# Performance work log

Measured on AMD Instinct MI355X. Metric: run time of the kernel, lower is better.

Reference implementation:

```python
import jax, jax.numpy as jnp
import numpy as np

B, N, F = 32, 64, 128   # batch, nodes, input features (F == hidden_dim)
E = N * (N - 1)         # fully-connected directed edges = 4032
H, D = 4, 64            # heads, out_dim per head
ALPHA = 0.2             # leaky relu slope


def setup_inputs() -> dict:
    key = jax.random.key(0)
    ks = jax.random.split(key, 16)
    v_self = jax.random.normal(ks[0], (B, N, F), dtype=jnp.float32)
    # fully-connected one-hot sender/receiver matrices [E, N], broadcast to [B, E, N]
    pairs = np.array([(i, j) for i in range(N) for j in range(N) if i != j])
    send = np.zeros((E, N), np.float32); send[np.arange(E), pairs[:, 0]] = 1.0
    rec = np.zeros((E, N), np.float32); rec[np.arange(E), pairs[:, 1]] = 1.0
    rel_send = jnp.broadcast_to(jnp.asarray(send), (B, E, N))
    rel_rec = jnp.broadcast_to(jnp.asarray(rec), (B, E, N))
    s = 0.05
    return {
        "v_self": v_self,
        "rel_rec": rel_rec,
        "rel_send": rel_send,
        "W_proj": jax.random.normal(ks[1], (H * D, F), dtype=jnp.float32) * s,
        "a_fwd": jax.random.normal(ks[2], (H, D), dtype=jnp.float32) * s,
        "a_bwd": jax.random.normal(ks[3], (H, D), dtype=jnp.float32) * s,
        "We1": jax.random.normal(ks[4], (D, 2 * D), dtype=jnp.float32) * s,
        "be1": jnp.zeros((D,), jnp.float32),
        "We2": jax.random.normal(ks[5], (D, D), dtype=jnp.float32) * s,
        "be2": jnp.zeros((D,), jnp.float32),
        "Wv1": jax.random.normal(ks[6], (F, D), dtype=jnp.float32) * s,
        "bv1": jnp.zeros((F,), jnp.float32),
        "Wv2": jax.random.normal(ks[7], (F, F), dtype=jnp.float32) * s,
        "bv2": jnp.zeros((F,), jnp.float32),
        "Wv3": jax.random.normal(ks[8], (D, F), dtype=jnp.float32) * s,
        "bv3": jnp.zeros((D,), jnp.float32),
    }


def _leaky(x):
    return jnp.where(x >= 0, x, ALPHA * x)


def reference(v_self, rel_rec, rel_send, W_proj, a_fwd, a_bwd,
              We1, be1, We2, be2, Wv1, bv1, Wv2, bv2, Wv3, bv3):
    # project: [B,N,F] -> [B,N,H,D]
    v_proj = (v_self @ W_proj.T).reshape(B, N, H, D)
    # gather to edges via one-hot adjacency (v_src==h_src, v_tgt==h_tgt in original)
    h_src = jnp.einsum('ben,bnhd->behd', rel_send, v_proj)
    h_tgt = jnp.einsum('ben,bnhd->behd', rel_rec, v_proj)
    attn_ij = _leaky(jnp.einsum('behd,hd->beh', h_src, a_fwd)) / 500.0
    attn_ji = _leaky(jnp.einsum('behd,hd->beh', h_tgt, a_bwd)) / 500.0
    attn_max = jnp.maximum(attn_ij, attn_ji)
    # NOTE: original applies exp twice (exp of exp); reproduced faithfully
    e_ij = jnp.exp(jnp.exp(attn_ij - attn_max))
    e_ji = jnp.exp(jnp.exp(attn_ji - attn_max))
    alpha_sum = e_ij + e_ji
    alpha_ij = e_ij / alpha_sum   # [B,E,H]
    alpha_ji = e_ji / alpha_sum
    edge_input = jnp.concatenate(
        [alpha_ij[..., None] * h_src, alpha_ji[..., None] * h_tgt], axis=-1)  # [B,E,H,2D]
    # f_CG_e: Linear(2D->D), ReLU, Linear(D->D) on last dim
    e_cg = jax.nn.relu(edge_input @ We1.T + be1) @ We2.T + be2
    edge_weighted = e_cg * alpha_ij[..., None]                               # [B,E,H,D]
    # scatter back to nodes
    v_social = jnp.einsum('behd,ben->bnhd', edge_weighted, rel_rec)          # [B,N,H,D]
    # f_CG_v: Linear(D->F), ReLU, Linear(F->F), ReLU, Linear(F->D)
    x = jax.nn.relu(v_social @ Wv1.T + bv1)
    x = jax.nn.relu(x @ Wv2.T + bv2)
    x = x @ Wv3.T + bv3
    v_out = x.reshape(B, N, H * D)  # concat_heads=True
    return (v_out, alpha_ij)
```

## Files before the change

kernel.cpp:

```cpp
#include <hip/hip_runtime.h>

#define B_ 32
#define N_ 64
#define F_ 128
#define E_ 4032
#define H_ 4
#define D_ 64

typedef __bf16 bf16x8 __attribute__((ext_vector_type(8)));
typedef __bf16 bf16x4 __attribute__((ext_vector_type(4)));
typedef float  f32x4  __attribute__((ext_vector_type(4)));


__global__ __launch_bounds__(256) void k_proj(
    const float* __restrict__ v_self, const float* __restrict__ W_proj,
    const float* __restrict__ We1,
    const float* __restrict__ a_fwd, const float* __restrict__ a_bwd,
    const float* __restrict__ Wv1, const float* __restrict__ We2,
    const float* __restrict__ be2, const float* __restrict__ Wv2,
    const float* __restrict__ Wv3,
    float* __restrict__ s_fwd, float* __restrict__ s_bwd,
    __bf16* __restrict__ u_src, __bf16* __restrict__ u_tgt,
    __bf16* __restrict__ M1bf, float* __restrict__ wb,
    __bf16* __restrict__ Wv2bf, __bf16* __restrict__ Wv3bf)
{
    const int t = threadIdx.x;

    if (blockIdx.x >= B_ * N_ / 8) {
        const int pid = (blockIdx.x - B_ * N_ / 8) * 256 + t;
        const int f = pid >> 6, k = pid & 63;
        float acc = 0.f;
        for (int dd = 0; dd < 64; ++dd)
            acc += Wv1[f * 64 + dd] * We2[dd * 64 + k];
        M1bf[pid] = (__bf16)acc;
        float p = Wv1[f * 64 + k] * be2[k];
#pragma unroll
        for (int m = 1; m < 64; m <<= 1) p += __shfl_xor(p, m);
        if (k == 0) wb[f] = p;
        Wv2bf[pid]        = (__bf16)Wv2[pid];
        Wv2bf[pid + 8192] = (__bf16)Wv2[pid + 8192];
        Wv3bf[pid]        = (__bf16)Wv3[pid];
        return;
    }

    const int w = t >> 6, l = t & 63;
    const int q = l >> 4, lr = l & 15;
    const int node0 = blockIdx.x * 8;

    __shared__ __bf16 Av[16 * 136];
    __shared__ __bf16 P_lds[8 * 288];

    {
        int row = t >> 5, c0 = (t & 31) * 4;
        float4 v = *(const float4*)(v_self + (size_t)(node0 + row) * 128 + c0);
        bf16x4 bv; bv[0]=(__bf16)v.x; bv[1]=(__bf16)v.y; bv[2]=(__bf16)v.z; bv[3]=(__bf16)v.w;
        *(bf16x4*)&Av[row * 136 + c0] = bv;
        bf16x4 z = {};
        *(bf16x4*)&Av[(row + 8) * 136 + c0] = z;
    }
    __syncthreads();

    f32x4 acc[4] = {};
#pragma unroll
    for (int ks = 0; ks < 4; ++ks) {
        bf16x8 a = *(const bf16x8*)&Av[lr * 136 + ks * 32 + q * 8];
#pragma unroll
        for (int ct = 0; ct < 4; ++ct) {
            const float4* wr = (const float4*)(W_proj + (size_t)(w * 64 + ct * 16 + lr) * 128 + ks * 32 + q * 8);
            float4 w0 = wr[0], w1 = wr[1];
            bf16x8 b;
            b[0]=(__bf16)w0.x; b[1]=(__bf16)w0.y; b[2]=(__bf16)w0.z; b[3]=(__bf16)w0.w;
            b[4]=(__bf16)w1.x; b[5]=(__bf16)w1.y; b[6]=(__bf16)w1.z; b[7]=(__bf16)w1.w;
            acc[ct] = __builtin_amdgcn_mfma_f32_16x16x32_bf16(a, b, acc[ct], 0, 0, 0);
        }
    }

    {
        float pf[4] = {0,0,0,0}, pb[4] = {0,0,0,0};
#pragma unroll
        for (int ct = 0; ct < 4; ++ct) {
            float af = a_fwd[w * 64 + ct * 16 + lr];
            float ab = a_bwd[w * 64 + ct * 16 + lr];
#pragma unroll
            for (int r = 0; r < 4; ++r) { pf[r] += acc[ct][r] * af; pb[r] += acc[ct][r] * ab; }
        }
#pragma unroll
        for (int m = 1; m < 16; m <<= 1) {
#pragma unroll
            for (int r = 0; r < 4; ++r) { pf[r] += __shfl_xor(pf[r], m); pb[r] += __shfl_xor(pb[r], m); }
        }
        if (lr == 0 && q < 2) {
#pragma unroll
            for (int r = 0; r < 4; ++r) {
                int node = q * 4 + r;
                float x = pf[r]; x = (x >= 0.f ? x : 0.2f * x) * 0.002f;
                float y = pb[r]; y = (y >= 0.f ? y : 0.2f * y) * 0.002f;
                s_fwd[(node0 + node) * 4 + w] = x;
                s_bwd[(node0 + node) * 4 + w] = y;
            }
        }
    }
    if (q < 2) {
#pragma unroll
        for (int ct = 0; ct < 4; ++ct)
#pragma unroll
            for (int r = 0; r < 4; ++r)
                P_lds[(q * 4 + r) * 288 + w * 72 + ct * 16 + lr] = (__bf16)acc[ct][r];
    }
    __syncthreads();

    const int rt = w & 1, mm = w >> 1;
    const int rr = rt * 16 + lr, an = rr >> 2, ah = rr & 3;
    f32x4 uacc[4] = {};
#pragma unroll
    for (int ks = 0; ks < 2; ++ks) {
        bf16x8 a = *(const bf16x8*)&P_lds[an * 288 + ah * 72 + ks * 32 + q * 8];
#pragma unroll
        for (int ct = 0; ct < 4; ++ct) {
            const float4* wr = (const float4*)(We1 + (size_t)(ct * 16 + lr) * 128 + mm * 64 + ks * 32 + q * 8);
            float4 w0 = wr[0], w1 = wr[1];
            bf16x8 b;
            b[0]=(__bf16)w0.x; b[1]=(__bf16)w0.y; b[2]=(__bf16)w0.z; b[3]=(__bf16)w0.w;
            b[4]=(__bf16)w1.x; b[5]=(__bf16)w1.y; b[6]=(__bf16)w1.z; b[7]=(__bf16)w1.w;
            uacc[ct] = __builtin_amdgcn_mfma_f32_16x16x32_bf16(a, b, uacc[ct], 0, 0, 0);
        }
    }
    __bf16* up = (mm == 0) ? u_src : u_tgt;
#pragma unroll
    for (int ct = 0; ct < 4; ++ct)
#pragma unroll
        for (int r = 0; r < 4; ++r) {
            int row = rt * 16 + q * 4 + r;
            up[(size_t)(node0 * 4 + row) * 64 + ct * 16 + lr] = (__bf16)uacc[ct][r];
        }
}

__global__ __launch_bounds__(256) void k_fused(
    const float* __restrict__ s_fwd, const float* __restrict__ s_bwd,
    const __bf16* __restrict__ u_src, const __bf16* __restrict__ u_tgt,
    const float* __restrict__ be1,
    const __bf16* __restrict__ M1bf, const float* __restrict__ wb,
    const float* __restrict__ bv1,
    const __bf16* __restrict__ Wv2bf, const float* __restrict__ bv2,
    const __bf16* __restrict__ Wv3bf, const float* __restrict__ bv3,
    float* __restrict__ v_out, float* __restrict__ out_alpha)
{
    const int t = threadIdx.x;
    const int h = t >> 6, d = t & 63;
    const int b = blockIdx.x >> 3, oct = blockIdx.x & 7;
    const int j0 = oct * 8;

    __shared__ float u_l[4][64][64];
    __shared__ float ut_l[8][4][64];
    __shared__ float aij_l[4][64][8];
    __shared__ float suma_l[32];
    __shared__ __bf16 g_l[32 * 72];

    {
        const __bf16* ub = u_src + (size_t)b * 16384;
        for (int idx = t * 8; idx < 16384; idx += 256 * 8) {
            bf16x8 v = *(const bf16x8*)(ub + idx);
            int i = idx >> 8, col = idx & 255;
            float* dst = &u_l[col >> 6][i][col & 63];
#pragma unroll
            for (int z = 0; z < 8; ++z) dst[z] = (float)v[z];
        }
        const __bf16* utp = u_tgt + ((size_t)(b * 64 + j0)) * 256;
        {
            int idx = t * 8;
            bf16x8 v = *(const bf16x8*)(utp + idx);
            int j = idx >> 8, col = idx & 255;
            float* dst = &ut_l[j][col >> 6][col & 63];
#pragma unroll
            for (int z = 0; z < 8; ++z) dst[z] = (float)v[z];
        }
    }

    {
        const int i = d;
        float sfi = s_fwd[(b * 64 + i) * 4 + h];
        float areg[8];
#pragma unroll
        for (int j = 0; j < 8; ++j) {
            float sbj = s_bwd[(b * 64 + j0 + j) * 4 + h];
            float m = fmaxf(sfi, sbj);
            float eij = __expf(__expf(sfi - m));
            float eji = __expf(__expf(sbj - m));
            float aij = eij / (eij + eji);
            if (i == j0 + j) aij = 0.f;
            areg[j] = aij;
        }
        f32x4 a0 = {areg[0], areg[1], areg[2], areg[3]};
        f32x4 a1 = {areg[4], areg[5], areg[6], areg[7]};
        *(f32x4*)&aij_l[h][i][0] = a0;
        *(f32x4*)&aij_l[h][i][4] = a1;
#pragma unroll
        for (int j = 0; j < 8; ++j) {
            float sa = areg[j];
#pragma unroll
            for (int m2 = 1; m2 < 64; m2 <<= 1) sa += __shfl_xor(sa, m2);
            if (i == 0) suma_l[j * 4 + h] = sa;
        }
    }
    if (t < 252) {
        const int jj = t >> 2, h2 = t & 3;
#pragma unroll
        for (int s = 0; s < 8; ++s) {
            int i2 = j0 + s;
            int j2 = jj + (jj >= i2 ? 1 : 0);
            float sfi = s_fwd[(b * 64 + i2) * 4 + h2];
            float sbj = s_bwd[(b * 64 + j2) * 4 + h2];
            float m = fmaxf(sfi, sbj);
            float eij = __expf(__expf(sfi - m));
            float eji = __expf(__expf(sbj - m));
            out_alpha[((size_t)b * E_ + i2 * 63 + jj) * 4 + h2] = eij / (eij + eji);
        }
    }
    __syncthreads();

    {
        const float be1d = be1[d];
        float utv[8], utb[8];
#pragma unroll
        for (int j = 0; j < 8; ++j) { utv[j] = ut_l[j][h][d]; utb[j] = utv[j] + be1d; }
        float gacc[8] = {};
        for (int i = 0; i < 64; ++i) {
            float usv = u_l[h][i][d];
            f32x4 a0 = *(const f32x4*)&aij_l[h][i][0];
            f32x4 a1 = *(const f32x4*)&aij_l[h][i][4];
#pragma unroll
            for (int j = 0; j < 4; ++j) {
                float a = a0[j];
                float hp = fmaf(a, usv - utv[j], utb[j]);
                gacc[j] = fmaf(a, fmaxf(hp, 0.f), gacc[j]);
                float a2 = a1[j];
                float hp2 = fmaf(a2, usv - utv[4 + j], utb[4 + j]);
                gacc[4 + j] = fmaf(a2, fmaxf(hp2, 0.f), gacc[4 + j]);
            }
        }
#pragma unroll
        for (int j = 0; j < 8; ++j)
            g_l[(j * 4 + h) * 72 + d] = (__bf16)gacc[j];
    }
    __syncthreads();

    __bf16* X1 = (__bf16*)&u_l[0][0][0];
    __bf16* X2 = X1 + 32 * 136;
    const int w = h, l = t & 63;
    const int q = l >> 4, lr = l & 15;
    const int rt = w & 1, ch = w >> 1;
    const int rows_base = (b * 64 + j0) * 4;

    f32x4 acc1[4] = {};
#pragma unroll
    for (int ks = 0; ks < 2; ++ks) {
        bf16x8 a = *(const bf16x8*)&g_l[(rt * 16 + lr) * 72 + ks * 32 + q * 8];
#pragma unroll
        for (int ct = 0; ct < 4; ++ct) {
            bf16x8 bfr = *(const bf16x8*)(M1bf + (size_t)(ch * 64 + ct * 16 + lr) * 64 + ks * 32 + q * 8);
            acc1[ct] = __builtin_amdgcn_mfma_f32_16x16x32_bf16(a, bfr, acc1[ct], 0, 0, 0);
        }
    }
    float sml[4];
#pragma unroll
    for (int r = 0; r < 4; ++r) sml[r] = suma_l[rt * 16 + q * 4 + r];
#pragma unroll
    for (int ct = 0; ct < 4; ++ct) {
        int f = ch * 64 + ct * 16 + lr;
        float wbf = wb[f], b1 = bv1[f];
#pragma unroll
        for (int r = 0; r < 4; ++r) {
            float xv = acc1[ct][r] + sml[r] * wbf + b1;
            X1[(rt * 16 + q * 4 + r) * 136 + f] = (__bf16)fmaxf(xv, 0.f);
        }
    }
    __syncthreads();

    f32x4 acc2[4] = {};
#pragma unroll
    for (int ks = 0; ks < 4; ++ks) {
        bf16x8 a = *(const bf16x8*)&X1[(rt * 16 + lr) * 136 + ks * 32 + q * 8];
#pragma unroll
        for (int ct = 0; ct < 4; ++ct) {
            bf16x8 bfr = *(const bf16x8*)(Wv2bf + (size_t)(ch * 64 + ct * 16 + lr) * 128 + ks * 32 + q * 8);
            acc2[ct] = __builtin_amdgcn_mfma_f32_16x16x32_bf16(a, bfr, acc2[ct], 0, 0, 0);
        }
    }
#pragma unroll
    for (int ct = 0; ct < 4; ++ct) {
        int f = ch * 64 + ct * 16 + lr;
        float b2 = bv2[f];
#pragma unroll
        for (int r = 0; r < 4; ++r) {
            float xv = acc2[ct][r] + b2;
            X2[(rt * 16 + q * 4 + r) * 136 + f] = (__bf16)fmaxf(xv, 0.f);
        }
    }
    __syncthreads();

    f32x4 acc3[2] = {};
#pragma unroll
    for (int ks = 0; ks < 4; ++ks) {
        bf16x8 a = *(const bf16x8*)&X2[(rt * 16 + lr) * 136 + ks * 32 + q * 8];
#pragma unroll
        for (int ct = 0; ct < 2; ++ct) {
            bf16x8 bfr = *(const bf16x8*)(Wv3bf + (size_t)(ch * 32 + ct * 16 + lr) * 128 + ks * 32 + q * 8);
            acc3[ct] = __builtin_amdgcn_mfma_f32_16x16x32_bf16(a, bfr, acc3[ct], 0, 0, 0);
        }
    }
#pragma unroll
    for (int ct = 0; ct < 2; ++ct) {
        int dd = ch * 32 + ct * 16 + lr;
        float b3 = bv3[dd];
#pragma unroll
        for (int r = 0; r < 4; ++r)
            v_out[(size_t)(rows_base + rt * 16 + q * 4 + r) * 64 + dd] = acc3[ct][r] + b3;
    }
}

extern "C" void kernel_launch(void* const* d_in, const int* in_sizes, int n_in,
                              void* d_out, int out_size, void* d_ws, size_t ws_size,
                              hipStream_t stream) {
    (void)in_sizes; (void)n_in; (void)out_size; (void)ws_size;
    const float* v_self = (const float*)d_in[0];
    const float* W_proj = (const float*)d_in[3];
    const float* a_fwd  = (const float*)d_in[4];
    const float* a_bwd  = (const float*)d_in[5];
    const float* We1    = (const float*)d_in[6];
    const float* be1    = (const float*)d_in[7];
    const float* We2    = (const float*)d_in[8];
    const float* be2    = (const float*)d_in[9];
    const float* Wv1    = (const float*)d_in[10];
    const float* bv1    = (const float*)d_in[11];
    const float* Wv2    = (const float*)d_in[12];
    const float* bv2    = (const float*)d_in[13];
    const float* Wv3    = (const float*)d_in[14];
    const float* bv3    = (const float*)d_in[15];

    float* ws = (float*)d_ws;
    float*  s_fwd = ws;
    float*  s_bwd = ws + 8192;
    float*  wb    = ws + 24576;
    __bf16* M1bf  = (__bf16*)(ws + 24704);
    __bf16* Wv2bf = (__bf16*)(ws + 28800);
    __bf16* Wv3bf = (__bf16*)(ws + 36992);
    __bf16* u_src = (__bf16*)(ws + 61568);
    __bf16* u_tgt = (__bf16*)(ws + 323712);

    float* v_out = (float*)d_out;
    float* alpha = v_out + (size_t)B_ * N_ * H_ * D_;

    hipLaunchKernelGGL(k_proj, dim3(B_ * N_ / 8 + 32), dim3(256), 0, stream,
                       v_self, W_proj, We1, a_fwd, a_bwd, Wv1, We2, be2, Wv2, Wv3,
                       s_fwd, s_bwd, u_src, u_tgt, M1bf, wb, Wv2bf, Wv3bf);
    hipLaunchKernelGGL(k_fused, dim3(B_ * N_ / 8), dim3(256), 0, stream,
                       s_fwd, s_bwd, u_src, u_tgt, be1, M1bf, wb, bv1,
                       Wv2bf, bv2, Wv3bf, bv3, v_out, alpha);
}
```

Before: 31.43 us.

## Repartition both kernels into smaller blocks and read u_src directly from global

k_proj now runs single-wave 64-thread blocks, each handling 16 nodes and one head. Each block computes both the u_src and u_tgt halves of We1, and the wasted zero-padded rows are dropped. k_fused handles 4 targets per block instead of 8, doubling the grid to 512 blocks, and streams u_src from global memory in bf16 instead of staging a 64 KB fp32 copy in LDS. The intent is to cut LDS use so more blocks fit per CU, and to fill the GPU better; the cost is redundant global reads of u_src across more blocks and less reuse per block.

Result: faster. 29.11 us (-7.4%).

```diff
diff --git a/kernel.cpp b/kernel.cpp
--- a/kernel.cpp
+++ b/kernel.cpp
@@ -12,7 +12,15 @@
 typedef float  f32x4  __attribute__((ext_vector_type(4)));
 
 
-__global__ __launch_bounds__(256) void k_proj(
+static __device__ inline bf16x8 ld_cvt8(const float* __restrict__ p) {
+    float4 w0 = *(const float4*)p, w1 = *(const float4*)(p + 4);
+    bf16x8 b;
+    b[0]=(__bf16)w0.x; b[1]=(__bf16)w0.y; b[2]=(__bf16)w0.z; b[3]=(__bf16)w0.w;
+    b[4]=(__bf16)w1.x; b[5]=(__bf16)w1.y; b[6]=(__bf16)w1.z; b[7]=(__bf16)w1.w;
+    return b;
+}
+
+__global__ __launch_bounds__(64) void k_proj(
     const float* __restrict__ v_self, const float* __restrict__ W_proj,
     const float* __restrict__ We1,
     const float* __restrict__ a_fwd, const float* __restrict__ a_bwd,
@@ -25,10 +33,12 @@
     __bf16* __restrict__ Wv2bf, __bf16* __restrict__ Wv3bf)
 {
     const int t = threadIdx.x;
-
-    if (blockIdx.x >= B_ * N_ / 8) {
-        const int pid = (blockIdx.x - B_ * N_ / 8) * 256 + t;
-        const int f = pid >> 6, k = pid & 63;
+    const int blk = blockIdx.x;
+
+    if (blk >= 512) {
+        const int f = blk - 512;
+        const int k = t;
+        const int pid = f * 64 + k;
         float acc = 0.f;
         for (int dd = 0; dd < 64; ++dd)
             acc += Wv1[f * 64 + dd] * We2[dd * 64 + k];
@@ -43,35 +53,20 @@
         return;
     }
 
-    const int w = t >> 6, l = t & 63;
-    const int q = l >> 4, lr = l & 15;
-    const int node0 = blockIdx.x * 8;
-
-    __shared__ __bf16 Av[16 * 136];
-    __shared__ __bf16 P_lds[8 * 288];
-
-    {
-        int row = t >> 5, c0 = (t & 31) * 4;
-        float4 v = *(const float4*)(v_self + (size_t)(node0 + row) * 128 + c0);
-        bf16x4 bv; bv[0]=(__bf16)v.x; bv[1]=(__bf16)v.y; bv[2]=(__bf16)v.z; bv[3]=(__bf16)v.w;
-        *(bf16x4*)&Av[row * 136 + c0] = bv;
-        bf16x4 z = {};
-        *(bf16x4*)&Av[(row + 8) * 136 + c0] = z;
-    }
-    __syncthreads();
+    const int tile = blk >> 2, w = blk & 3;
+    const int node0 = tile * 16;
+    const int q = t >> 4, lr = t & 15;
+
+    __shared__ __bf16 P_lds[16 * 72];
 
     f32x4 acc[4] = {};
 #pragma unroll
     for (int ks = 0; ks < 4; ++ks) {
-        bf16x8 a = *(const bf16x8*)&Av[lr * 136 + ks * 32 + q * 8];
+        bf16x8 a = ld_cvt8(v_self + (size_t)(node0 + lr) * 128 + ks * 32 + q * 8);
 #pragma unroll
         for (int ct = 0; ct < 4; ++ct) {
-            const float4* wr = (const float4*)(W_proj + (size_t)(w * 64 + ct * 16 + lr) * 128 + ks * 32 + q * 8);
-            float4 w0 = wr[0], w1 = wr[1];
-            bf16x8 b;
-            b[0]=(__bf16)w0.x; b[1]=(__bf16)w0.y; b[2]=(__bf16)w0.z; b[3]=(__bf16)w0.w;
-            b[4]=(__bf16)w1.x; b[5]=(__bf16)w1.y; b[6]=(__bf16)w1.z; b[7]=(__bf16)w1.w;
-            acc[ct] = __builtin_amdgcn_mfma_f32_16x16x32_bf16(a, b, acc[ct], 0, 0, 0);
+            bf16x8 bb = ld_cvt8(W_proj + (size_t)(w * 64 + ct * 16 + lr) * 128 + ks * 32 + q * 8);
+            acc[ct] = __builtin_amdgcn_mfma_f32_16x16x32_bf16(a, bb, acc[ct], 0, 0, 0);
         }
     }
 
@@ -89,49 +84,43 @@
 #pragma unroll
             for (int r = 0; r < 4; ++r) { pf[r] += __shfl_xor(pf[r], m); pb[r] += __shfl_xor(pb[r], m); }
         }
-        if (lr == 0 && q < 2) {
+        if (lr == 0) {
 #pragma unroll
             for (int r = 0; r < 4; ++r) {
-                int node = q * 4 + r;
                 float x = pf[r]; x = (x >= 0.f ? x : 0.2f * x) * 0.002f;
                 float y = pb[r]; y = (y >= 0.f ? y : 0.2f * y) * 0.002f;
-                s_fwd[(node0 + node) * 4 + w] = x;
-                s_bwd[(node0 + node) * 4 + w] = y;
+                s_fwd[(node0 + q * 4 + r) * 4 + w] = x;
+                s_bwd[(node0 + q * 4 + r) * 4 + w] = y;
             }
         }
     }
-    if (q < 2) {
-#pragma unroll
-        for (int ct = 0; ct < 4; ++ct)
-#pragma unroll
-            for (int r = 0; r < 4; ++r)
-                P_lds[(q * 4 + r) * 288 + w * 72 + ct * 16 + lr] = (__bf16)acc[ct][r];
-    }
-    __syncthreads();
-
-    const int rt = w & 1, mm = w >> 1;
-    const int rr = rt * 16 + lr, an = rr >> 2, ah = rr & 3;
-    f32x4 uacc[4] = {};
+
+#pragma unroll
+    for (int ct = 0; ct < 4; ++ct)
+#pragma unroll
+        for (int r = 0; r < 4; ++r)
+            P_lds[(q * 4 + r) * 72 + ct * 16 + lr] = (__bf16)acc[ct][r];
+    __syncthreads();
+
+    f32x4 us[4] = {}, ut[4] = {};
 #pragma unroll
     for (int ks = 0; ks < 2; ++ks) {
-        bf16x8 a = *(const bf16x8*)&P_lds[an * 288 + ah * 72 + ks * 32 + q * 8];
+        bf16x8 a = *(const bf16x8*)&P_lds[lr * 72 + ks * 32 + q * 8];
 #pragma unroll
         for (int ct = 0; ct < 4; ++ct) {
-            const float4* wr = (const float4*)(We1 + (size_t)(ct * 16 + lr) * 128 + mm * 64 + ks * 32 + q * 8);
-            float4 w0 = wr[0], w1 = wr[1];
-            bf16x8 b;
-            b[0]=(__bf16)w0.x; b[1]=(__bf16)w0.y; b[2]=(__bf16)w0.z; b[3]=(__bf16)w0.w;
-            b[4]=(__bf16)w1.x; b[5]=(__bf16)w1.y; b[6]=(__bf16)w1.z; b[7]=(__bf16)w1.w;
-            uacc[ct] = __builtin_amdgcn_mfma_f32_16x16x32_bf16(a, b, uacc[ct], 0, 0, 0);
-        }
-    }
-    __bf16* up = (mm == 0) ? u_src : u_tgt;
+            bf16x8 bs = ld_cvt8(We1 + (size_t)(ct * 16 + lr) * 128 + ks * 32 + q * 8);
+            us[ct] = __builtin_amdgcn_mfma_f32_16x16x32_bf16(a, bs, us[ct], 0, 0, 0);
+            bf16x8 bt = ld_cvt8(We1 + (size_t)(ct * 16 + lr) * 128 + 64 + ks * 32 + q * 8);
+            ut[ct] = __builtin_amdgcn_mfma_f32_16x16x32_bf16(a, bt, ut[ct], 0, 0, 0);
+        }
+    }
 #pragma unroll
     for (int ct = 0; ct < 4; ++ct)
 #pragma unroll
         for (int r = 0; r < 4; ++r) {
-            int row = rt * 16 + q * 4 + r;
-            up[(size_t)(node0 * 4 + row) * 64 + ct * 16 + lr] = (__bf16)uacc[ct][r];
+            size_t row = (size_t)(node0 + q * 4 + r) * 4 + w;
+            u_src[row * 64 + ct * 16 + lr] = (__bf16)us[ct][r];
+            u_tgt[row * 64 + ct * 16 + lr] = (__bf16)ut[ct][r];
         }
 }
 
@@ -147,65 +136,54 @@
 {
     const int t = threadIdx.x;
     const int h = t >> 6, d = t & 63;
-    const int b = blockIdx.x >> 3, oct = blockIdx.x & 7;
-    const int j0 = oct * 8;
-
-    __shared__ float u_l[4][64][64];
-    __shared__ float ut_l[8][4][64];
-    __shared__ float aij_l[4][64][8];
-    __shared__ float suma_l[32];
-    __shared__ __bf16 g_l[32 * 72];
-
-    {
-        const __bf16* ub = u_src + (size_t)b * 16384;
-        for (int idx = t * 8; idx < 16384; idx += 256 * 8) {
-            bf16x8 v = *(const bf16x8*)(ub + idx);
-            int i = idx >> 8, col = idx & 255;
-            float* dst = &u_l[col >> 6][i][col & 63];
-#pragma unroll
-            for (int z = 0; z < 8; ++z) dst[z] = (float)v[z];
-        }
-        const __bf16* utp = u_tgt + ((size_t)(b * 64 + j0)) * 256;
-        {
-            int idx = t * 8;
-            bf16x8 v = *(const bf16x8*)(utp + idx);
-            int j = idx >> 8, col = idx & 255;
-            float* dst = &ut_l[j][col >> 6][col & 63];
-#pragma unroll
-            for (int z = 0; z < 8; ++z) dst[z] = (float)v[z];
-        }
+    const int b = blockIdx.x >> 4, quad = blockIdx.x & 15;
+    const int j0 = quad * 4;
+
+    __shared__ float  ut_l[4][4][64];
+    __shared__ float  aij_l[4][64][4];
+    __shared__ float  suma_l[16];
+    __shared__ __bf16 g_l[16 * 72];
+    __shared__ __bf16 X1[16 * 136];
+    __shared__ __bf16 X2[16 * 136];
+
+    {
+        int idx = t * 4;
+        bf16x4 v = *(const bf16x4*)(u_tgt + (size_t)(b * 64 + j0) * 256 + idx);
+        int j = idx >> 8, col = idx & 255;
+        f32x4 f;
+#pragma unroll
+        for (int z = 0; z < 4; ++z) f[z] = (float)v[z];
+        *(f32x4*)&ut_l[j][col >> 6][col & 63] = f;
     }
 
     {
         const int i = d;
         float sfi = s_fwd[(b * 64 + i) * 4 + h];
-        float areg[8];
-#pragma unroll
-        for (int j = 0; j < 8; ++j) {
-            float sbj = s_bwd[(b * 64 + j0 + j) * 4 + h];
+        float areg[4];
+#pragma unroll
+        for (int jl = 0; jl < 4; ++jl) {
+            float sbj = s_bwd[(b * 64 + j0 + jl) * 4 + h];
             float m = fmaxf(sfi, sbj);
             float eij = __expf(__expf(sfi - m));
             float eji = __expf(__expf(sbj - m));
             float aij = eij / (eij + eji);
-            if (i == j0 + j) aij = 0.f;
-            areg[j] = aij;
-        }
-        f32x4 a0 = {areg[0], areg[1], areg[2], areg[3]};
-        f32x4 a1 = {areg[4], areg[5], areg[6], areg[7]};
-        *(f32x4*)&aij_l[h][i][0] = a0;
-        *(f32x4*)&aij_l[h][i][4] = a1;
-#pragma unroll
-        for (int j = 0; j < 8; ++j) {
-            float sa = areg[j];
+            if (i == j0 + jl) aij = 0.f;
+            areg[jl] = aij;
+        }
+        f32x4 a4 = {areg[0], areg[1], areg[2], areg[3]};
+        *(f32x4*)&aij_l[h][i][0] = a4;
+#pragma unroll
+        for (int jl = 0; jl < 4; ++jl) {
+            float sa = areg[jl];
 #pragma unroll
             for (int m2 = 1; m2 < 64; m2 <<= 1) sa += __shfl_xor(sa, m2);
-            if (i == 0) suma_l[j * 4 + h] = sa;
+            if (i == 0) suma_l[jl * 4 + h] = sa;
         }
     }
     if (t < 252) {
         const int jj = t >> 2, h2 = t & 3;
 #pragma unroll
-        for (int s = 0; s < 8; ++s) {
+        for (int s = 0; s < 4; ++s) {
             int i2 = j0 + s;
             int j2 = jj + (jj >= i2 ? 1 : 0);
             float sfi = s_fwd[(b * 64 + i2) * 4 + h2];
@@ -220,101 +198,94 @@
 
     {
         const float be1d = be1[d];
-        float utv[8], utb[8];
-#pragma unroll
-        for (int j = 0; j < 8; ++j) { utv[j] = ut_l[j][h][d]; utb[j] = utv[j] + be1d; }
-        float gacc[8] = {};
+        float utv[4], utb[4];
+#pragma unroll
+        for (int jl = 0; jl < 4; ++jl) { utv[jl] = ut_l[jl][h][d]; utb[jl] = utv[jl] + be1d; }
+        float gacc[4] = {};
+        const __bf16* usp = u_src + ((size_t)(b * 64) * 4 + h) * 64 + d;
+#pragma unroll 4
         for (int i = 0; i < 64; ++i) {
-            float usv = u_l[h][i][d];
-            f32x4 a0 = *(const f32x4*)&aij_l[h][i][0];
-            f32x4 a1 = *(const f32x4*)&aij_l[h][i][4];
-#pragma unroll
-            for (int j = 0; j < 4; ++j) {
-                float a = a0[j];
-                float hp = fmaf(a, usv - utv[j], utb[j]);
-                gacc[j] = fmaf(a, fmaxf(hp, 0.f), gacc[j]);
-                float a2 = a1[j];
-                float hp2 = fmaf(a2, usv - utv[4 + j], utb[4 + j]);
-                gacc[4 + j] = fmaf(a2, fmaxf(hp2, 0.f), gacc[4 + j]);
+            float usv = (float)usp[i * 256];
+            f32x4 a4 = *(const f32x4*)&aij_l[h][i][0];
+#pragma unroll
+            for (int jl = 0; jl < 4; ++jl) {
+                float a = a4[jl];
+                float hp = fmaf(a, usv - utv[jl], utb[jl]);
+                gacc[jl] = fmaf(a, fmaxf(hp, 0.f), gacc[jl]);
             }
         }
 #pragma unroll
-        for (int j = 0; j < 8; ++j)
-            g_l[(j * 4 + h) * 72 + d] = (__bf16)gacc[j];
-    }
-    __syncthreads();
-
-    __bf16* X1 = (__bf16*)&u_l[0][0][0];
-    __bf16* X2 = X1 + 32 * 136;
-    const int w = h, l = t & 63;
-    const int q = l >> 4, lr = l & 15;
-    const int rt = w & 1, ch = w >> 1;
-    const int rows_base = (b * 64 + j0) * 4;
-
-    f32x4 acc1[4] = {};
+        for (int jl = 0; jl < 4; ++jl)
+            g_l[(jl * 4 + h) * 72 + d] = (__bf16)gacc[jl];
+    }
+    __syncthreads();
+
+    const int w = h;
+    const int q = d >> 4, lr = d & 15;
+
+    f32x4 acc1[2] = {};
 #pragma unroll
     for (int ks = 0; ks < 2; ++ks) {
-        bf16x8 a = *(const bf16x8*)&g_l[(rt * 16 + lr) * 72 + ks * 32 + q * 8];
-#pragma unroll
-        for (int ct = 0; ct < 4; ++ct) {
-            bf16x8 bfr = *(const bf16x8*)(M1bf + (size_t)(ch * 64 + ct * 16 + lr) * 64 + ks * 32 + q * 8);
-            acc1[ct] = __builtin_amdgcn_mfma_f32_16x16x32_bf16(a, bfr, acc1[ct], 0, 0, 0);
+        bf16x8 a = *(const bf16x8*)&g_l[lr * 72 + ks * 32 + q * 8];
+#pragma unroll
+        for (int c = 0; c < 2; ++c) {
+            int ct = w * 2 + c;
+            bf16x8 bb = *(const bf16x8*)(M1bf + (size_t)(ct * 16 + lr) * 64 + ks * 32 + q * 8);
+            acc1[c] = __builtin_amdgcn_mfma_f32_16x16x32_bf16(a, bb, acc1[c], 0, 0, 0);
         }
     }
     float sml[4];
 #pragma unroll
-    for (int r = 0; r < 4; ++r) sml[r] = suma_l[rt * 16 + q * 4 + r];
-#pragma unroll
-    for (int ct = 0; ct < 4; ++ct) {
-        int f = ch * 64 + ct * 16 + lr;
+    for (int r = 0; r < 4; ++r) sml[r] = suma_l[q * 4 + r];
+#pragma unroll
+    for (int c = 0; c < 2; ++c) {
+        int f = (w * 2 + c) * 16 + lr;
         float wbf = wb[f], b1 = bv1[f];
 #pragma unroll
         for (int r = 0; r < 4; ++r) {
-            float xv = acc1[ct][r] + sml[r] * wbf + b1;
-            X1[(rt * 16 + q * 4 + r) * 136 + f] = (__bf16)fmaxf(xv, 0.f);
-        }
-    }
-    __syncthreads();
-
-    f32x4 acc2[4] = {};
+            float xv = acc1[c][r] + sml[r] * wbf + b1;
+            X1[(q * 4 + r) * 136 + f] = (__bf16)fmaxf(xv, 0.f);
+        }
+    }
+    __syncthreads();
+
+    f32x4 acc2[2] = {};
 #pragma unroll
     for (int ks = 0; ks < 4; ++ks) {
-        bf16x8 a = *(const bf16x8*)&X1[(rt * 16 + lr) * 136 + ks * 32 + q * 8];
-#pragma unroll
-        for (int ct = 0; ct < 4; ++ct) {
-            bf16x8 bfr = *(const bf16x8*)(Wv2bf + (size_t)(ch * 64 + ct * 16 + lr) * 128 + ks * 32 + q * 8);
-            acc2[ct] = __builtin_amdgcn_mfma_f32_16x16x32_bf16(a, bfr, acc2[ct], 0, 0, 0);
-        }
-    }
-#pragma unroll
-    for (int ct = 0; ct < 4; ++ct) {
-        int f = ch * 64 + ct * 16 + lr;
+        bf16x8 a = *(const bf16x8*)&X1[lr * 136 + ks * 32 + q * 8];
+#pragma unroll
+        for (int c = 0; c < 2; ++c) {
+            int ct = w * 2 + c;
+            bf16x8 bb = *(const bf16x8*)(Wv2bf + (size_t)(ct * 16 + lr) * 128 + ks * 32 + q * 8);
+            acc2[c] = __builtin_amdgcn_mfma_f32_16x16x32_bf16(a, bb, acc2[c], 0, 0, 0);
+        }
+    }
+#pragma unroll
+    for (int c = 0; c < 2; ++c) {
+        int f = (w * 2 + c) * 16 + lr;
         float b2 = bv2[f];
 #pragma unroll
         for (int r = 0; r < 4; ++r) {
-            float xv = acc2[ct][r] + b2;
-            X2[(rt * 16 + q * 4 + r) * 136 + f] = (__bf16)fmaxf(xv, 0.f);
-        }
-    }
-    __syncthreads();
-
-    f32x4 acc3[2] = {};
+            float xv = acc2[c][r] + b2;
+            X2[(q * 4 + r) * 136 + f] = (__bf16)fmaxf(xv, 0.f);
+        }
+    }
+    __syncthreads();
+
+    f32x4 acc3 = {};
 #pragma unroll
     for (int ks = 0; ks < 4; ++ks) {
-        bf16x8 a = *(const bf16x8*)&X2[(rt * 16 + lr) * 136 + ks * 32 + q * 8];
-#pragma unroll
-        for (int ct = 0; ct < 2; ++ct) {
-            bf16x8 bfr = *(const bf16x8*)(Wv3bf + (size_t)(ch * 32 + ct * 16 + lr) * 128 + ks * 32 + q * 8);
-            acc3[ct] = __builtin_amdgcn_mfma_f32_16x16x32_bf16(a, bfr, acc3[ct], 0, 0, 0);
-        }
-    }
-#pragma unroll
-    for (int ct = 0; ct < 2; ++ct) {
-        int dd = ch * 32 + ct * 16 + lr;
+        bf16x8 a = *(const bf16x8*)&X2[lr * 136 + ks * 32 + q * 8];
+        bf16x8 bb = *(const bf16x8*)(Wv3bf + (size_t)(w * 16 + lr) * 128 + ks * 32 + q * 8);
+        acc3 = __builtin_amdgcn_mfma_f32_16x16x32_bf16(a, bb, acc3, 0, 0, 0);
+    }
+    {
+        int dd = w * 16 + lr;
         float b3 = bv3[dd];
+        size_t rows_base = (size_t)(b * 64 + j0) * 4;
 #pragma unroll
         for (int r = 0; r < 4; ++r)
-            v_out[(size_t)(rows_base + rt * 16 + q * 4 + r) * 64 + dd] = acc3[ct][r] + b3;
+            v_out[(rows_base + q * 4 + r) * 64 + dd] = acc3[r] + b3;
     }
 }
 
@@ -350,10 +321,10 @@
     float* v_out = (float*)d_out;
     float* alpha = v_out + (size_t)B_ * N_ * H_ * D_;
 
-    hipLaunchKernelGGL(k_proj, dim3(B_ * N_ / 8 + 32), dim3(256), 0, stream,
+    hipLaunchKernelGGL(k_proj, dim3(512 + 128), dim3(64), 0, stream,
                        v_self, W_proj, We1, a_fwd, a_bwd, Wv1, We2, be2, Wv2, Wv3,
                        s_fwd, s_bwd, u_src, u_tgt, M1bf, wb, Wv2bf, Wv3bf);
-    hipLaunchKernelGGL(k_fused, dim3(B_ * N_ / 8), dim3(256), 0, stream,
+    hipLaunchKernelGGL(k_fused, dim3(B_ * N_ / 4), dim3(256), 0, stream,
                        s_fwd, s_bwd, u_src, u_tgt, be1, M1bf, wb, bv1,
                        Wv2bf, bv2, Wv3bf, bv3, v_out, alpha);
 }
```
